# Kernel optimization log

Measured on AMD Instinct MI355X. Metric: run time of the kernel, lower is better.

The kernel has to match this reference:

```python
import jax, jax.numpy as jnp
import numpy as np

EPS = 1e-6

def rms_norm(x):
    return x * jax.lax.rsqrt(jnp.mean(x * x, axis=-1, keepdims=True) + EPS)

def setup_inputs() -> dict:
    key = jax.random.key(0)
    k_x, k_w = jax.random.split(key)
    T, B, D = 2048, 16, 1024
    x = jax.random.normal(k_x, (T, B, D), dtype=jnp.float32)
    h0 = jnp.zeros((B, D), dtype=jnp.float32)
    # xavier_uniform for W: limit = sqrt(6/(fan_in+fan_out)) = sqrt(6/(2D))
    limit = float(np.sqrt(6.0 / (2 * D)))
    W = jax.random.uniform(k_w, (D, D), dtype=jnp.float32, minval=-limit, maxval=limit)
    b = jnp.zeros((D,), dtype=jnp.float32)
    log_alpha = jnp.asarray(np.log(0.1), dtype=jnp.float32)
    return {"x": x, "h0": h0, "W": W, "b": b, "log_alpha": log_alpha}

def reference(x, h0, W, b, log_alpha):
    # x: [T,B,D], h0: [B,D], W: [D,D], b: [D], log_alpha: []
    alpha = jnp.exp(log_alpha)
    # Precompute all input projections in one big GEMM: [T,B,D]
    Wx_all = jnp.einsum('tbd,ed->tbe', x, W) + b

    def step(h, wx):
        h_new = rms_norm(h + alpha * wx)
        out = h_new * jax.nn.silu(h_new)
        return h_new, (h_new, out)

    _, (hs, outs) = jax.lax.scan(step, h0, Wx_all)
    h = jnp.concatenate([h0[None], hs], axis=0)  # [T+1,B,D]
    return outs, h
```

## Files before the change

kernel.cpp:

```cpp
#include <hip/hip_runtime.h>
#include <hip/hip_bf16.h>

#define T_STEPS 2048
#define BATCH 16
#define DIM 1024
#define EPSV 1e-6f
#define INVD (1.0f / 1024.0f)
#define SLOTF (BATCH * DIM)
#define SLOT4C (BATCH * DIM / 4)

typedef short short8 __attribute__((ext_vector_type(8)));
typedef float f32x4 __attribute__((ext_vector_type(4)));

struct alignas(16) bf16x8pack { __hip_bfloat16 v[8]; };

__device__ __forceinline__ float dot4(const float4& a, const float4& c) {
  return fmaf(a.x, c.x, fmaf(a.y, c.y, fmaf(a.z, c.z, a.w * c.w)));
}
__device__ __forceinline__ float fast_rsq(float x) {
  float r;
  asm("v_rsq_f32 %0, %1" : "=v"(r) : "v"(x));
  return r;
}

__global__ __launch_bounds__(256) void cvt_kernel(const float* __restrict__ xsrc,
                                                  const float* __restrict__ wsrc,
                                                  bf16x8pack* __restrict__ xdst,
                                                  bf16x8pack* __restrict__ wdst,
                                                  int nx8, int ntot8) {
  int i = blockIdx.x * blockDim.x + threadIdx.x;
  if (i >= ntot8) return;
  const float* src;
  bf16x8pack* dst;
  int k;
  if (i < nx8) { src = xsrc; dst = xdst; k = i; }
  else         { src = wsrc; dst = wdst; k = i - nx8; }
  const float4* s4 = (const float4*)src + (size_t)k * 2;
  float4 a = s4[0];
  float4 b = s4[1];
  bf16x8pack p;
  p.v[0] = __float2bfloat16(a.x); p.v[1] = __float2bfloat16(a.y);
  p.v[2] = __float2bfloat16(a.z); p.v[3] = __float2bfloat16(a.w);
  p.v[4] = __float2bfloat16(b.x); p.v[5] = __float2bfloat16(b.y);
  p.v[6] = __float2bfloat16(b.z); p.v[7] = __float2bfloat16(b.w);
  dst[k] = p;
}

__global__ __launch_bounds__(256) void gemm_kernel(
    const __hip_bfloat16* __restrict__ Xb,
    const __hip_bfloat16* __restrict__ Wb,
    const float* __restrict__ bias,
    const float* __restrict__ log_alpha_p,
    float* __restrict__ hreg) {
  __shared__ __hip_bfloat16 As[128 * 32];
  __shared__ __hip_bfloat16 Bs[128 * 32];
  const int tid = threadIdx.x;
  const int wave = tid >> 6, lane = tid & 63;
  const int d = blockIdx.x;
  const int work = ((d & 7) << 8) + (d >> 3);
  const int m0 = (work >> 3) * 128;
  const int e0 = (work & 7) * 128;
  const int wm = (wave >> 1) * 64;
  const int wn = (wave & 1) * 64;
  const int l15 = lane & 15, l4 = lane >> 4;

  f32x4 acc[4][4] = {};

  const int srow = wave * 16 + (lane >> 2);
  const int sch = (lane & 3) * 8;

  for (int kt = 0; kt < DIM; kt += 32) {
    __syncthreads();
#pragma unroll
    for (int i = 0; i < 2; ++i) {
      const __hip_bfloat16* ga = Xb + (size_t)(m0 + i * 64 + srow) * DIM + kt + sch;
      const __hip_bfloat16* gb = Wb + (size_t)(e0 + i * 64 + srow) * DIM + kt + sch;
      __builtin_amdgcn_global_load_lds(
          (const __attribute__((address_space(1))) void*)ga,
          (__attribute__((address_space(3))) void*)((char*)As + (i * 64 + wave * 16) * 64),
          16, 0, 0);
      __builtin_amdgcn_global_load_lds(
          (const __attribute__((address_space(1))) void*)gb,
          (__attribute__((address_space(3))) void*)((char*)Bs + (i * 64 + wave * 16) * 64),
          16, 0, 0);
    }
    __syncthreads();
    short8 a[4], b[4];
#pragma unroll
    for (int f = 0; f < 4; ++f)
      a[f] = *(const short8*)((const char*)As + ((wm + f * 16 + l15) * 32 + l4 * 8) * 2);
#pragma unroll
    for (int g = 0; g < 4; ++g)
      b[g] = *(const short8*)((const char*)Bs + ((wn + g * 16 + l15) * 32 + l4 * 8) * 2);
#pragma unroll
    for (int f = 0; f < 4; ++f)
#pragma unroll
      for (int g = 0; g < 4; ++g)
        acc[f][g] = __builtin_amdgcn_mfma_f32_16x16x32_bf16(a[f], b[g], acc[f][g], 0, 0, 0);
  }
  const float alpha = __expf(log_alpha_p[0]);
#pragma unroll
  for (int g = 0; g < 4; ++g) {
    const int e = e0 + wn + g * 16 + l15;
    const float bv = bias[e];
#pragma unroll
    for (int f = 0; f < 4; ++f) {
#pragma unroll
      for (int r = 0; r < 4; ++r) {
        const int m = m0 + wm + f * 16 + l4 * 4 + r;
        hreg[(size_t)(m + BATCH) * DIM + e] = alpha * (acc[f][g][r] + bv);
      }
    }
  }
}

__device__ __forceinline__ float dpp_sum_reg(float x) {
  float acc = x;
#define DPP_ADD(ctrl)                                                              \
  {                                                                                \
    int t_ = __builtin_amdgcn_update_dpp(0, __float_as_int(acc), (ctrl), 0xf, 0xf, \
                                         true);                                    \
    acc += __int_as_float(t_);                                                     \
  }
  DPP_ADD(0x111); DPP_ADD(0x112); DPP_ADD(0x114); DPP_ADD(0x118);
  DPP_ADD(0x142); DPP_ADD(0x143);
#undef DPP_ADD
  return acc;
}

__global__ __launch_bounds__(64, 1) void dots_kernel(const float* __restrict__ hreg,
                                                     float4* __restrict__ scal4,
                                                     float2* __restrict__ d45g) {
  const int tile = blockIdx.x >> 4;
  const int b = blockIdx.x & 15;
  const int t0 = tile * 8;
  const int lane = threadIdx.x;
  const float4* h4 = (const float4*)hreg;

  float4 R[13][4];
#pragma unroll
  for (int k = 0; k < 13; ++k) {
    int si = t0 - 4 + k;
    if (si < 0) si = 0;
#pragma unroll
    for (int j = 0; j < 4; ++j)
      R[k][j] = h4[(size_t)si * SLOT4C + b * 256 + lane + 64 * j];
  }

#pragma unroll
  for (int u = 0; u < 8; ++u) {
    const int t = t0 + u;
    float e = 0.f, d = 0.f, d2 = 0.f, d3 = 0.f, d4 = 0.f, d5 = 0.f;
#pragma unroll
    for (int j = 0; j < 4; ++j) {
      const float4 a = R[u + 5][j];
      e = fmaf(a.x, a.x, fmaf(a.y, a.y, fmaf(a.z, a.z, fmaf(a.w, a.w, e))));
      const float4 p1 = R[u + 4][j];
      d = fmaf(p1.x, a.x, fmaf(p1.y, a.y, fmaf(p1.z, a.z, fmaf(p1.w, a.w, d))));
      const float4 p2 = R[u + 3][j];
      d2 = fmaf(p2.x, a.x, fmaf(p2.y, a.y, fmaf(p2.z, a.z, fmaf(p2.w, a.w, d2))));
      const float4 p3 = R[u + 2][j];
      d3 = fmaf(p3.x, a.x, fmaf(p3.y, a.y, fmaf(p3.z, a.z, fmaf(p3.w, a.w, d3))));
      const float4 p4 = R[u + 1][j];
      d4 = fmaf(p4.x, a.x, fmaf(p4.y, a.y, fmaf(p4.z, a.z, fmaf(p4.w, a.w, d4))));
      const float4 p5 = R[u][j];
      d5 = fmaf(p5.x, a.x, fmaf(p5.y, a.y, fmaf(p5.z, a.z, fmaf(p5.w, a.w, d5))));
    }
    e = dpp_sum_reg(e);
    d = dpp_sum_reg(d);
    d2 = dpp_sum_reg(d2);
    d3 = dpp_sum_reg(d3);
    d4 = dpp_sum_reg(d4);
    d5 = dpp_sum_reg(d5);
    if (lane == 63) {
      const float dd  = (t >= 1) ? d + d : 0.f;
      const float dd2 = (t >= 2) ? d2 + d2 : 0.f;
      const float dd3 = (t >= 3) ? d3 + d3 : 0.f;
      const float dd4 = (t >= 4) ? d4 + d4 : 0.f;
      const float dd5 = (t >= 5) ? d5 + d5 : 0.f;
      scal4[b * T_STEPS + t] = make_float4(e, dd, dd2, dd3);
      d45g[b * T_STEPS + t] = make_float2(dd4, dd5);
    }
  }
}

__global__ __launch_bounds__(256, 1) void scan_kernel(
    const float* __restrict__ h0,
    const float4* __restrict__ scal4,
    const float2* __restrict__ d45g,
    float* __restrict__ hreg) {
  const int b = blockIdx.x;
  const int tid = threadIdx.x;
  const int wave = tid >> 6;
  const int lane = tid & 63;
  float4* h4 = (float4*)hreg;
  const int idx4 = b * 256 + tid;

  __shared__ float4 scLDS[T_STEPS];
  __shared__ float2 d45LDS[T_STEPS];
  __shared__ alignas(16) float Gp[4][4];
  __shared__ float initP[4][6];

#pragma unroll
  for (int p = 0; p < 8; ++p)
    scLDS[p * 256 + tid] = scal4[b * T_STEPS + p * 256 + tid];
#pragma unroll
  for (int p = 0; p < 8; ++p)
    d45LDS[p * 256 + tid] = d45g[b * T_STEPS + p * 256 + tid];

  float4 w[16];
#pragma unroll
  for (int k = 2; k < 16; ++k) w[k] = h4[(size_t)SLOT4C * (k + 1) + idx4];
  w[0] = h4[(size_t)SLOT4C * 17 + idx4];
  w[1] = h4[(size_t)SLOT4C * 18 + idx4];
  float4 w0v = h4[(size_t)SLOT4C * 1 + idx4];
  float4 w1v = h4[(size_t)SLOT4C * 2 + idx4];
  float4 h0v = ((const float4*)h0)[idx4];
  h4[idx4] = h0v;

  float4 s;
  s.x = h0v.x + w0v.x; s.y = h0v.y + w0v.y;
  s.z = h0v.z + w0v.z; s.w = h0v.w + w0v.w;
  {
    float q  = dpp_sum_reg(dot4(s, s));
    float r  = dpp_sum_reg(dot4(s, w1v));
    float c2 = dpp_sum_reg(dot4(s, w[2]));
    float c3 = dpp_sum_reg(dot4(s, w[3]));
    float c4 = dpp_sum_reg(dot4(s, w[4]));
    float c5 = dpp_sum_reg(dot4(s, w[5]));
    if (lane == 63) {
      initP[wave][0] = q;  initP[wave][1] = r;  initP[wave][2] = c2;
      initP[wave][3] = c3; initP[wave][4] = c4; initP[wave][5] = c5;
    }
  }
  __syncthreads();
  const float n1 = (initP[0][0] + initP[1][0]) + (initP[2][0] + initP[3][0]);
  float t1 = (initP[0][1] + initP[1][1]) + (initP[2][1] + initP[3][1]);
  float t2 = (initP[0][2] + initP[1][2]) + (initP[2][2] + initP[3][2]);
  float t3 = (initP[0][3] + initP[1][3]) + (initP[2][3] + initP[3][3]);
  float t4 = (initP[0][4] + initP[1][4]) + (initP[2][4] + initP[3][4]);
  float t5 = (initP[0][5] + initP[1][5]) + (initP[2][5] + initP[3][5]);
  const float B1 = t1 + t1, C2 = t2 + t2, C3 = t3 + t3, C4 = t4 + t4, C5 = t5 + t5;

  const float e1 = scLDS[1].x;
  float4 sc2 = scLDS[2], sc3 = scLDS[3], sc4 = scLDS[4], sc5 = scLDS[5];
  const float D45x = d45LDS[5].x;
  float4 scA = scLDS[6], scB = scLDS[7];
  float2 d45A = d45LDS[6], d45B = d45LDS[7];

  float n = n1, rm1, rm2, rm3, rm4, pp;
  float gr0 = 0.f, gr1 = 0.f;
  float4 rv = make_float4(0.f, 0.f, 0.f, 0.f);
  float4 hvr[4];

#define BAR0 { asm volatile("s_waitcnt lgkmcnt(0)" ::: "memory"); __builtin_amdgcn_s_barrier(); }

  {
    const float rinv = fast_rsq(fmaf(n, INVD, EPSV));
    n = fmaf(rinv, fmaf(rinv, n, B1), e1);
    hvr[1].x = rinv * s.x; hvr[1].y = rinv * s.y;
    hvr[1].z = rinv * s.z; hvr[1].w = rinv * s.w;
    h4[(size_t)SLOT4C * 1 + idx4] = hvr[1];
    s.x = hvr[1].x + w1v.x; s.y = hvr[1].y + w1v.y;
    s.z = hvr[1].z + w1v.z; s.w = hvr[1].w + w1v.w;
    pp = dpp_sum_reg(dot4(hvr[1], w[6]));
    rm1 = rinv;
    BAR0
  }
  {
    if (lane == 63) Gp[2][wave] = pp;
    const float rinv = fast_rsq(fmaf(n, INVD, EPSV));
    const float BB = fmaf(rm1, C2, sc2.y);
    n = fmaf(rinv, fmaf(rinv, n, BB), sc2.x);
    hvr[2].x = rinv * s.x; hvr[2].y = rinv * s.y;
    hvr[2].z = rinv * s.z; hvr[2].w = rinv * s.w;
    h4[(size_t)SLOT4C * 2 + idx4] = hvr[2];
    s.x = hvr[2].x + w[2].x; s.y = hvr[2].y + w[2].y;
    s.z = hvr[2].z + w[2].z; s.w = hvr[2].w + w[2].w;
    pp = dpp_sum_reg(dot4(hvr[2], w[7]));
    w[2] = h4[(size_t)SLOT4C * 19 + idx4];
    rm2 = rm1; rm1 = rinv;
    BAR0
  }
  {
    if (lane == 63) Gp[3][wave] = pp;
    const float rinv = fast_rsq(fmaf(n, INVD, EPSV));
    const float BB = fmaf(rm1, fmaf(rm2, C3, sc3.z), sc3.y);
    n = fmaf(rinv, fmaf(rinv, n, BB), sc3.x);
    hvr[3].x = rinv * s.x; hvr[3].y = rinv * s.y;
    hvr[3].z = rinv * s.z; hvr[3].w = rinv * s.w;
    h4[(size_t)SLOT4C * 3 + idx4] = hvr[3];
    s.x = hvr[3].x + w[3].x; s.y = hvr[3].y + w[3].y;
    s.z = hvr[3].z + w[3].z; s.w = hvr[3].w + w[3].w;
    pp = dpp_sum_reg(dot4(hvr[3], w[8]));
    w[3] = h4[(size_t)SLOT4C * 20 + idx4];
    rm3 = rm2; rm2 = rm1; rm1 = rinv;
    BAR0
  }
  {
    if (lane == 63) Gp[0][wave] = pp;
    const float rinv = fast_rsq(fmaf(n, INVD, EPSV));
    const float BB = fmaf(rm1, fmaf(rm2, fmaf(rm3, C4, sc4.w), sc4.z), sc4.y);
    n = fmaf(rinv, fmaf(rinv, n, BB), sc4.x);
    rv = *(const float4*)&Gp[2][0];
    hvr[0].x = rinv * s.x; hvr[0].y = rinv * s.y;
    hvr[0].z = rinv * s.z; hvr[0].w = rinv * s.w;
    h4[(size_t)SLOT4C * 4 + idx4] = hvr[0];
    s.x = hvr[0].x + w[4].x; s.y = hvr[0].y + w[4].y;
    s.z = hvr[0].z + w[4].z; s.w = hvr[0].w + w[4].w;
    pp = dpp_sum_reg(dot4(hvr[0], w[9]));
    w[4] = h4[(size_t)SLOT4C * 21 + idx4];
    rm4 = rm3; rm3 = rm2; rm2 = rm1; rm1 = rinv;
    BAR0
  }
  {
    if (lane == 63) Gp[1][wave] = pp;
    const float rinv = fast_rsq(fmaf(n, INVD, EPSV));
    const float BB =
        fmaf(rm1, fmaf(rm2, fmaf(rm3, fmaf(rm4, C5, D45x), sc5.w), sc5.z), sc5.y);
    n = fmaf(rinv, fmaf(rinv, n, BB), sc5.x);
    { float gt = (rv.x + rv.y) + (rv.z + rv.w); gr0 = gt + gt; }
    rv = *(const float4*)&Gp[3][0];
    hvr[1].x = rinv * s.x; hvr[1].y = rinv * s.y;
    hvr[1].z = rinv * s.z; hvr[1].w = rinv * s.w;
    h4[(size_t)SLOT4C * 5 + idx4] = hvr[1];
    s.x = hvr[1].x + w[5].x; s.y = hvr[1].y + w[5].y;
    s.z = hvr[1].z + w[5].z; s.w = hvr[1].w + w[5].w;
    pp = dpp_sum_reg(dot4(hvr[1], w[10]));
    w[5] = h4[(size_t)SLOT4C * 22 + idx4];
    rm4 = rm3; rm3 = rm2; rm2 = rm1; rm1 = rinv;
    BAR0
  }

#define STEP(I_, WS, W5S, GW, GR, SCR, D45R, GRU, GRW, HVI, BAR_)                    \
  {                                                                                  \
    const int i_ = (I_);                                                             \
    if (lane == 63) Gp[GW][wave] = pp;                                               \
    { float gt_ = (rv.x + rv.y) + (rv.z + rv.w); GRW = gt_ + gt_; }                  \
    rv = *(const float4*)&Gp[GR][0];                                                 \
    const float rinv = fast_rsq(fmaf(n, INVD, EPSV));                                \
    const float BB = fmaf(                                                           \
        rm1, fmaf(rm2, fmaf(rm3, fmaf(rm4, (D45R).y + (GRU), (D45R).x), (SCR).w),    \
                  (SCR).z), (SCR).y);                                                \
    n = fmaf(rinv, fmaf(rinv, n, BB), (SCR).x);                                      \
    hvr[HVI].x = rinv * s.x; hvr[HVI].y = rinv * s.y;                                \
    hvr[HVI].z = rinv * s.z; hvr[HVI].w = rinv * s.w;                                \
    h4[(size_t)SLOT4C * i_ + idx4] = hvr[HVI];                                       \
    s.x = hvr[HVI].x + w[WS].x; s.y = hvr[HVI].y + w[WS].y;                          \
    s.z = hvr[HVI].z + w[WS].z; s.w = hvr[HVI].w + w[WS].w;                          \
    pp = dpp_sum_reg(dot4(hvr[HVI], w[W5S]));                                        \
    const int ipf_ = (i_ + 16 < T_STEPS) ? (i_ + 16) : (T_STEPS - 1);                \
    w[WS] = h4[(size_t)SLOT4C * (ipf_ + 1) + idx4];                                  \
    const int isc_ = (i_ + 2 < T_STEPS) ? (i_ + 2) : (T_STEPS - 1);                  \
    SCR = scLDS[isc_];                                                               \
    D45R = d45LDS[isc_];                                                             \
    rm4 = rm3; rm3 = rm2; rm2 = rm1; rm1 = rinv;                                     \
    if (BAR_) { asm volatile("s_waitcnt lgkmcnt(3)" ::: "memory");                   \
                __builtin_amdgcn_s_barrier(); }                                      \
  }

  for (int ii = 6; ii < 2038; ii += 16) {
    STEP(ii + 0,  6, 11, 2, 0, scA, d45A, gr0, gr1, 2, 0)
    STEP(ii + 1,  7, 12, 3, 1, scB, d45B, gr1, gr0, 3, 1)
    STEP(ii + 2,  8, 13, 0, 2, scA, d45A, gr0, gr1, 0, 0)
    STEP(ii + 3,  9, 14, 1, 3, scB, d45B, gr1, gr0, 1, 1)
    STEP(ii + 4, 10, 15, 2, 0, scA, d45A, gr0, gr1, 2, 0)
    STEP(ii + 5, 11,  0, 3, 1, scB, d45B, gr1, gr0, 3, 1)
    STEP(ii + 6, 12,  1, 0, 2, scA, d45A, gr0, gr1, 0, 0)
    STEP(ii + 7, 13,  2, 1, 3, scB, d45B, gr1, gr0, 1, 1)
    STEP(ii + 8, 14,  3, 2, 0, scA, d45A, gr0, gr1, 2, 0)
    STEP(ii + 9, 15,  4, 3, 1, scB, d45B, gr1, gr0, 3, 1)
    STEP(ii + 10, 0,  5, 0, 2, scA, d45A, gr0, gr1, 0, 0)
    STEP(ii + 11, 1,  6, 1, 3, scB, d45B, gr1, gr0, 1, 1)
    STEP(ii + 12, 2,  7, 2, 0, scA, d45A, gr0, gr1, 2, 0)
    STEP(ii + 13, 3,  8, 3, 1, scB, d45B, gr1, gr0, 3, 1)
    STEP(ii + 14, 4,  9, 0, 2, scA, d45A, gr0, gr1, 0, 0)
    STEP(ii + 15, 5, 10, 1, 3, scB, d45B, gr1, gr0, 1, 1)
  }
  STEP(2038,  6, 11, 2, 0, scA, d45A, gr0, gr1, 2, 0)
  STEP(2039,  7, 12, 3, 1, scB, d45B, gr1, gr0, 3, 1)
  STEP(2040,  8, 13, 0, 2, scA, d45A, gr0, gr1, 0, 0)
  STEP(2041,  9, 14, 1, 3, scB, d45B, gr1, gr0, 1, 1)
  STEP(2042, 10, 15, 2, 0, scA, d45A, gr0, gr1, 2, 0)
  STEP(2043, 11,  0, 3, 1, scB, d45B, gr1, gr0, 3, 1)
  STEP(2044, 12,  1, 0, 2, scA, d45A, gr0, gr1, 0, 0)
  STEP(2045, 13,  2, 1, 3, scB, d45B, gr1, gr0, 1, 1)
  STEP(2046, 14,  3, 2, 0, scA, d45A, gr0, gr1, 2, 0)
  STEP(2047, 15,  4, 3, 1, scB, d45B, gr1, gr0, 3, 1)
#undef STEP
#undef BAR0

  const float rinvT = fast_rsq(fmaf(n, INVD, EPSV));
  float4 o;
  o.x = rinvT * s.x; o.y = rinvT * s.y; o.z = rinvT * s.z; o.w = rinvT * s.w;
  h4[(size_t)SLOT4C * T_STEPS + idx4] = o;
}

__global__ __launch_bounds__(256) void silu_kernel(const float4* __restrict__ hsrc,
                                                   float4* __restrict__ out4, int n4) {
  for (int i = blockIdx.x * 256 + threadIdx.x; i < n4; i += 2048 * 256) {
    float4 h = hsrc[i];
    float4 o;
    o.x = h.x * h.x / (1.f + __expf(-h.x));
    o.y = h.y * h.y / (1.f + __expf(-h.y));
    o.z = h.z * h.z / (1.f + __expf(-h.z));
    o.w = h.w * h.w / (1.f + __expf(-h.w));
    out4[i] = o;
  }
}

extern "C" void kernel_launch(void* const* d_in, const int* in_sizes, int n_in,
                              void* d_out, int out_size, void* d_ws, size_t ws_size,
                              hipStream_t stream) {
  (void)in_sizes; (void)n_in; (void)d_ws; (void)ws_size; (void)out_size;
  const float* x = (const float*)d_in[0];
  const float* h0 = (const float*)d_in[1];
  const float* W = (const float*)d_in[2];
  const float* bias = (const float*)d_in[3];
  const float* log_alpha = (const float*)d_in[4];

  float* out = (float*)d_out;
  float* hreg = out + (size_t)T_STEPS * BATCH * DIM;
  __hip_bfloat16* xb = (__hip_bfloat16*)d_out;
  __hip_bfloat16* wb = (__hip_bfloat16*)((char*)d_out + (size_t)T_STEPS * BATCH * DIM * 2);
  float4* scal4 = (float4*)(out + (size_t)26 * 1024 * 1024);
  float2* d45g = (float2*)(out + (size_t)27 * 1024 * 1024);

  const int nx8 = T_STEPS * BATCH * DIM / 8;
  const int nw8 = DIM * DIM / 8;
  const int ntot8 = nx8 + nw8;
  cvt_kernel<<<(ntot8 + 255) / 256, 256, 0, stream>>>(x, W, (bf16x8pack*)xb,
                                                      (bf16x8pack*)wb, nx8, ntot8);

  gemm_kernel<<<2048, 256, 0, stream>>>(xb, wb, bias, log_alpha, hreg);

  dots_kernel<<<(T_STEPS / 8) * BATCH, 64, 0, stream>>>(hreg, scal4, d45g);

  scan_kernel<<<BATCH, 256, 0, stream>>>(h0, scal4, d45g, hreg);

  const int n4 = T_STEPS * BATCH * DIM / 4;
  silu_kernel<<<2048, 256, 0, stream>>>((const float4*)(hreg + BATCH * DIM),
                                        (float4*)out, n4);
}
```

Baseline: 511.7 us.

## Rewrite GEMM with 256x256 tiles, 4-stage LDS pipeline and swizzled loads

Replaces the 128x128 single-buffered GEMM with 256x256 tiles per 512-thread block. It uses a 4-slot LDS ring fed by global_load_lds prefetching two k-steps ahead, an XOR swizzle to avoid LDS bank conflicts, and split A/B staging phases with setprio around the MFMA bursts. The goal is to hide global load latency and raise MFMA utilisation in the projection GEMM. In exchange the kernel uses 128KB of LDS, larger accumulators and more complex barrier choreography, which limits occupancy to one block per CU.

```diff
diff --git a/kernel.cpp b/kernel.cpp
--- a/kernel.cpp
+++ b/kernel.cpp
@@ -46,68 +46,122 @@
   dst[k] = p;
 }
 
-__global__ __launch_bounds__(256) void gemm_kernel(
+__global__ __launch_bounds__(512, 1) void gemm_kernel(
     const __hip_bfloat16* __restrict__ Xb,
     const __hip_bfloat16* __restrict__ Wb,
     const float* __restrict__ bias,
     const float* __restrict__ log_alpha_p,
     float* __restrict__ hreg) {
-  __shared__ __hip_bfloat16 As[128 * 32];
-  __shared__ __hip_bfloat16 Bs[128 * 32];
+  __shared__ char lds[4 * 32768];
   const int tid = threadIdx.x;
-  const int wave = tid >> 6, lane = tid & 63;
+  const int w = tid >> 6, l = tid & 63;
   const int d = blockIdx.x;
-  const int work = ((d & 7) << 8) + (d >> 3);
-  const int m0 = (work >> 3) * 128;
-  const int e0 = (work & 7) * 128;
-  const int wm = (wave >> 1) * 64;
-  const int wn = (wave & 1) * 64;
-  const int l15 = lane & 15, l4 = lane >> 4;
-
-  f32x4 acc[4][4] = {};
-
-  const int srow = wave * 16 + (lane >> 2);
-  const int sch = (lane & 3) * 8;
-
-  for (int kt = 0; kt < DIM; kt += 32) {
-    __syncthreads();
-#pragma unroll
-    for (int i = 0; i < 2; ++i) {
-      const __hip_bfloat16* ga = Xb + (size_t)(m0 + i * 64 + srow) * DIM + kt + sch;
-      const __hip_bfloat16* gb = Wb + (size_t)(e0 + i * 64 + srow) * DIM + kt + sch;
-      __builtin_amdgcn_global_load_lds(
-          (const __attribute__((address_space(1))) void*)ga,
-          (__attribute__((address_space(3))) void*)((char*)As + (i * 64 + wave * 16) * 64),
-          16, 0, 0);
-      __builtin_amdgcn_global_load_lds(
-          (const __attribute__((address_space(1))) void*)gb,
-          (__attribute__((address_space(3))) void*)((char*)Bs + (i * 64 + wave * 16) * 64),
-          16, 0, 0);
-    }
-    __syncthreads();
-    short8 a[4], b[4];
-#pragma unroll
-    for (int f = 0; f < 4; ++f)
-      a[f] = *(const short8*)((const char*)As + ((wm + f * 16 + l15) * 32 + l4 * 8) * 2);
-#pragma unroll
-    for (int g = 0; g < 4; ++g)
-      b[g] = *(const short8*)((const char*)Bs + ((wn + g * 16 + l15) * 32 + l4 * 8) * 2);
-#pragma unroll
-    for (int f = 0; f < 4; ++f)
-#pragma unroll
-      for (int g = 0; g < 4; ++g)
-        acc[f][g] = __builtin_amdgcn_mfma_f32_16x16x32_bf16(a[f], b[g], acc[f][g], 0, 0, 0);
-  }
+  const int work = ((d & 7) << 6) + (d >> 3);
+  const int mt = work >> 2;
+  const int et = work & 3;
+  const int wr = w >> 2, wc = w & 3;
+  const int l15 = l & 15, l4 = l >> 4;
+
+  f32x4 acc[8][4] = {};
+
+  const int srow = w * 16 + (l >> 2);
+  const int scol = 8 * ((l & 3) ^ ((l >> 2) & 3));
+  const int kxor = (l4 * 16) ^ ((l & 3) << 4);
+
+  const __hip_bfloat16* Abase = Xb + (size_t)(mt * 256 + srow) * DIM + scol;
+  const __hip_bfloat16* Bbase = Wb + (size_t)(et * 256 + srow) * DIM + scol;
+
+#define GLD1(GSRC, LOFF)                                                           \
+  __builtin_amdgcn_global_load_lds(                                                \
+      (const __attribute__((address_space(1))) void*)(GSRC),                       \
+      (__attribute__((address_space(3))) void*)(lds + (LOFF)), 16, 0, 0)
+#define STAGE_A(SLOT, KT)                                                          \
+  GLD1(Abase + (KT), (SLOT) * 32768 + w * 1024);                                   \
+  GLD1(Abase + (KT) + 128 * DIM, (SLOT) * 32768 + 8192 + w * 1024);
+#define STAGE_B(SLOT, KT)                                                          \
+  GLD1(Bbase + (KT), (SLOT) * 32768 + 16384 + w * 1024);                           \
+  GLD1(Bbase + (KT) + 128 * DIM, (SLOT) * 32768 + 16384 + 8192 + w * 1024);
+
+  STAGE_A(0, 0) STAGE_B(0, 0)
+  STAGE_A(1, 32) STAGE_B(1, 32)
+  asm volatile("s_waitcnt vmcnt(0)" ::: "memory");
+  __builtin_amdgcn_s_barrier();
+
+  short8 a_[4], b_[4];
+
+#define PH1(SL, STSL, STKT, DOST)                                                  \
+  {                                                                                \
+    asm volatile("s_waitcnt vmcnt(4)" ::: "memory");                               \
+    __builtin_amdgcn_sched_barrier(0);                                             \
+    const char* As_ = lds + (SL) * 32768;                                          \
+    const char* Bs_ = As_ + 16384;                                                 \
+    _Pragma("unroll")                                                              \
+    for (int f = 0; f < 4; ++f)                                                    \
+      a_[f] = *(const short8*)(As_ + (wr * 128 + f * 16 + l15) * 64 + kxor);       \
+    _Pragma("unroll")                                                              \
+    for (int g = 0; g < 4; ++g)                                                    \
+      b_[g] = *(const short8*)(Bs_ + (wc * 64 + g * 16 + l15) * 64 + kxor);        \
+    if (DOST) { STAGE_A(STSL, STKT) }                                              \
+    __builtin_amdgcn_s_barrier();                                                  \
+    asm volatile("s_waitcnt lgkmcnt(0)" ::: "memory");                             \
+    __builtin_amdgcn_sched_barrier(0);                                             \
+    __builtin_amdgcn_s_setprio(1);                                                 \
+    _Pragma("unroll")                                                              \
+    for (int f = 0; f < 4; ++f)                                                    \
+      _Pragma("unroll")                                                            \
+      for (int g = 0; g < 4; ++g)                                                  \
+        acc[f][g] = __builtin_amdgcn_mfma_f32_16x16x32_bf16(a_[f], b_[g],          \
+                                                            acc[f][g], 0, 0, 0);  \
+    __builtin_amdgcn_s_setprio(0);                                                 \
+    __builtin_amdgcn_s_barrier();                                                  \
+  }
+#define PH2(SL, STSL, STKT, DOST)                                                  \
+  {                                                                                \
+    const char* As_ = lds + (SL) * 32768;                                          \
+    _Pragma("unroll")                                                              \
+    for (int f = 0; f < 4; ++f)                                                    \
+      a_[f] = *(const short8*)(As_ + (wr * 128 + (f + 4) * 16 + l15) * 64 + kxor); \
+    if (DOST) { STAGE_B(STSL, STKT) }                                              \
+    __builtin_amdgcn_s_barrier();                                                  \
+    asm volatile("s_waitcnt lgkmcnt(0)" ::: "memory");                             \
+    __builtin_amdgcn_sched_barrier(0);                                             \
+    __builtin_amdgcn_s_setprio(1);                                                 \
+    _Pragma("unroll")                                                              \
+    for (int f = 0; f < 4; ++f)                                                    \
+      _Pragma("unroll")                                                            \
+      for (int g = 0; g < 4; ++g)                                                  \
+        acc[f + 4][g] = __builtin_amdgcn_mfma_f32_16x16x32_bf16(a_[f], b_[g],      \
+                                                                acc[f + 4][g],    \
+                                                                0, 0, 0);         \
+    __builtin_amdgcn_s_setprio(0);                                                 \
+    __builtin_amdgcn_s_barrier();                                                  \
+  }
+
+  for (int k = 0; k < 30; ++k) {
+    const int sl = k & 3;
+    const int st = (k + 2) & 3;
+    const int stkt = (k + 2) * 32;
+    PH1(sl, st, stkt, 1)
+    PH2(sl, st, stkt, 1)
+  }
+  PH1(2, 0, 0, 0) PH2(2, 0, 0, 0)
+  PH1(3, 0, 0, 0) PH2(3, 0, 0, 0)
+#undef PH1
+#undef PH2
+#undef STAGE_A
+#undef STAGE_B
+#undef GLD1
+
   const float alpha = __expf(log_alpha_p[0]);
 #pragma unroll
   for (int g = 0; g < 4; ++g) {
-    const int e = e0 + wn + g * 16 + l15;
+    const int e = et * 256 + wc * 64 + g * 16 + l15;
     const float bv = bias[e];
 #pragma unroll
-    for (int f = 0; f < 4; ++f) {
+    for (int f = 0; f < 8; ++f) {
 #pragma unroll
       for (int r = 0; r < 4; ++r) {
-        const int m = m0 + wm + f * 16 + l4 * 4 + r;
+        const int m = mt * 256 + wr * 128 + f * 16 + l4 * 4 + r;
         hreg[(size_t)(m + BATCH) * DIM + e] = alpha * (acc[f][g][r] + bv);
       }
     }
@@ -432,7 +486,7 @@
   cvt_kernel<<<(ntot8 + 255) / 256, 256, 0, stream>>>(x, W, (bf16x8pack*)xb,
                                                       (bf16x8pack*)wb, nx8, ntot8);
 
-  gemm_kernel<<<2048, 256, 0, stream>>>(xb, wb, bias, log_alpha, hreg);
+  gemm_kernel<<<512, 512, 0, stream>>>(xb, wb, bias, log_alpha, hreg);
 
   dots_kernel<<<(T_STEPS / 8) * BATCH, 64, 0, stream>>>(hreg, scal4, d45g);
 
```

Result: no change. 503.7 us (-1.6%).
